# Performance work log

Measured on AMD Instinct MI355X. Metric: run time of the kernel, lower is better.

Reference implementation:

```python
import jax, jax.numpy as jnp
import numpy as np

SLOPE = 0.2
NEG = -9e15

def setup_inputs() -> dict:
    key = jax.random.key(0)
    k1, k2, k3, k4 = jax.random.split(key, 4)
    N, INP, OUT = 8192, 512, 128
    h = jax.random.normal(k1, (N, INP), dtype=jnp.float32)
    adj = jax.random.randint(k2, (N, N), 0, 2, dtype=jnp.int32)
    W = jax.random.normal(k3, (INP, OUT), dtype=jnp.float32) * (1.0 / np.sqrt(INP))
    a = jax.random.normal(k4, (2 * OUT,), dtype=jnp.float32) * (1.0 / np.sqrt(2 * OUT))
    return {"h": h, "adj": adj, "W": W, "a": a}

def reference(h, adj, W, a):
    OUT = W.shape[1]
    Wh = h @ W                               # [N, out]
    # a . [Wh_i, Wh_j] decomposes into two matvecs (same math as pairwise concat)
    f1 = Wh @ a[:OUT]                        # [N]
    f2 = Wh @ a[OUT:]                        # [N]
    e = jax.nn.leaky_relu(f1[:, None] + f2[None, :], negative_slope=SLOPE)  # [N, N]
    scores = jnp.where(adj > 0, e, NEG)
    attention = jax.nn.softmax(scores, axis=1)
    return attention @ Wh                    # [N, out]
```

## Files before the change

kernel.cpp:

```cpp
#include <hip/hip_runtime.h>

typedef unsigned short u16;
typedef __attribute__((ext_vector_type(8))) short short8v;
typedef __attribute__((ext_vector_type(4))) short short4v;
typedef __attribute__((ext_vector_type(4))) float float4v;
typedef __attribute__((ext_vector_type(4))) int   int4v;

#define N_NODES 8192
#define D_IN    512
#define D_OUT   128
#define SLOPEF  0.2f
#define NSEG    4
#define SEGCOLS 2048
#define NCHUNK  8

static __device__ __forceinline__ float bf2f(u16 u) {
    union { unsigned int i; float f; } v; v.i = ((unsigned int)u) << 16; return v.f;
}
static __device__ __forceinline__ u16 f2bf(float f) {
    union { float f; unsigned int i; } v; v.f = f;
    unsigned int r = v.i + 0x7fff + ((v.i >> 16) & 1);
    return (u16)(r >> 16);
}
static __device__ __forceinline__ void lds_barrier() {
    asm volatile("s_waitcnt lgkmcnt(0)" ::: "memory");
    __builtin_amdgcn_s_barrier();
    asm volatile("" ::: "memory");
}

__global__ __launch_bounds__(256, 2) void k1_proj(
        const float* __restrict__ h, const float* __restrict__ W,
        const float* __restrict__ a, u16* __restrict__ WhT,
        float* __restrict__ f1, float* __restrict__ f2)
{
    __shared__ float hs[16 * D_IN];
    __shared__ float buf[16 * 128];
    __shared__ float part[16][17];
    const int tid = threadIdx.x;
    const int rowbase = blockIdx.x * 16;

    const float4v* hsrc = (const float4v*)(h + (size_t)rowbase * D_IN);
    #pragma unroll
    for (int i = 0; i < 8; i++) {
        *(float4v*)&hs[(tid + 256 * i) * 4] = hsrc[tid + 256 * i];
    }
    __syncthreads();

    const int c  = tid & 127;
    const int rh = tid >> 7;
    float acc[8];
    #pragma unroll
    for (int rr = 0; rr < 8; rr++) acc[rr] = 0.f;

    for (int k = 0; k < D_IN; k += 4) {
        float wv[4];
        #pragma unroll
        for (int kk = 0; kk < 4; kk++) wv[kk] = W[(k + kk) * D_OUT + c];
        #pragma unroll
        for (int rr = 0; rr < 8; rr++) {
            float4v hv = *(const float4v*)&hs[(rh * 8 + rr) * D_IN + k];
            acc[rr] += hv[0] * wv[0];
            acc[rr] += hv[1] * wv[1];
            acc[rr] += hv[2] * wv[2];
            acc[rr] += hv[3] * wv[3];
        }
    }

    {
        short8v pack;
        #pragma unroll
        for (int rr = 0; rr < 8; rr++) pack[rr] = (short)f2bf(acc[rr]);
        *(short8v*)(WhT + (size_t)c * N_NODES + rowbase + rh * 8) = pack;
    }

    const float a1 = a[c];
    const float a2 = a[D_OUT + c];

    #pragma unroll
    for (int rr = 0; rr < 8; rr++) buf[(rh * 8 + rr) * 128 + c] = acc[rr] * a1;
    __syncthreads();
    {
        const int row = tid >> 4, seg = tid & 15;
        float p = 0.f;
        #pragma unroll
        for (int e = 0; e < 8; e++) p += buf[row * 128 + seg * 8 + e];
        part[row][seg] = p;
    }
    __syncthreads();
    if (tid < 16) {
        float s = 0.f;
        #pragma unroll
        for (int j = 0; j < 16; j++) s += part[tid][j];
        f1[rowbase + tid] = s;
    }
    __syncthreads();
    #pragma unroll
    for (int rr = 0; rr < 8; rr++) buf[(rh * 8 + rr) * 128 + c] = acc[rr] * a2;
    __syncthreads();
    {
        const int row = tid >> 4, seg = tid & 15;
        float p = 0.f;
        #pragma unroll
        for (int e = 0; e < 8; e++) p += buf[row * 128 + seg * 8 + e];
        part[row][seg] = p;
    }
    __syncthreads();
    if (tid < 16) {
        float s = 0.f;
        #pragma unroll
        for (int j = 0; j < 16; j++) s += part[tid][j];
        f2[rowbase + tid] = s;
    }
}

__global__ __launch_bounds__(256, 4) void k2_attn(
        const int* __restrict__ adj, const u16* __restrict__ WhT,
        const float* __restrict__ f1g, const float* __restrict__ f2g,
        float* __restrict__ numw, float* __restrict__ denw)
{
    __shared__ short Pt[32 * 264];
    __shared__ float f2s[SEGCOLS];
    __shared__ float f1s[32];
    __shared__ float rs[32][9];
    __shared__ float ssum[32];

    const int tid = threadIdx.x;
    const int rb  = blockIdx.x >> 2;
    const int seg = blockIdx.x & 3;
    const int rowbase = rb * 32;
    const int colbase = seg * SEGCOLS;
    const int r = tid >> 3, g = tid & 7;
    const int lane = tid & 63, w = tid >> 6;
    const int quad = lane >> 4, m16 = lane & 15;

    if (tid < 32) f1s[tid] = f1g[rowbase + tid];
    #pragma unroll
    for (int i = 0; i < 2; i++)
        *(float4v*)&f2s[(tid + 256 * i) * 4] = *(const float4v*)&f2g[colbase + (tid + 256 * i) * 4];

    const int4v* arow = (const int4v*)(adj + (size_t)(rowbase + r) * N_NODES + colbase);
    int4v a4[8];
    #pragma unroll
    for (int i = 0; i < 8; i++) a4[i] = arow[g + 8 * i];

    float4v acc[2][2];
    #pragma unroll
    for (int mt = 0; mt < 2; mt++)
        #pragma unroll
        for (int nt = 0; nt < 2; nt++) {
            acc[mt][nt][0] = 0.f; acc[mt][nt][1] = 0.f;
            acc[mt][nt][2] = 0.f; acc[mt][nt][3] = 0.f;
        }
    float lsum = 0.f;

    __syncthreads();

    for (int jc = 0; jc < NCHUNK; jc++) {
        const float f1v = f1s[r];
        #pragma unroll
        for (int i = 0; i < 8; i++) {
            const int c0 = (g + 8 * i) * 4;
            const float4v fv = *(const float4v*)&f2s[jc * 256 + c0];
            const int4v av = a4[i];
            short4v pv;
            #pragma unroll
            for (int e = 0; e < 4; e++) {
                float x = f1v + fv[e];
                x = fmaxf(x, SLOPEF * x);
                const float wv = (av[e] > 0) ? __expf(x) : 0.f;
                const u16 wb = f2bf(wv);
                lsum += bf2f(wb);
                pv[e] = (short)wb;
            }
            *(short4v*)&Pt[r * 264 + c0] = pv;
        }
        if (jc + 1 < NCHUNK) {
            #pragma unroll
            for (int i = 0; i < 8; i++) a4[i] = arow[(jc + 1) * 64 + g + 8 * i];
        }
        lds_barrier();

        {
            const u16* b0p = WhT + (size_t)(w * 32 + m16) * N_NODES + colbase + jc * 256 + quad * 8;
            const u16* b1p = b0p + 16 * N_NODES;
            const short* a0p = &Pt[m16 * 264 + quad * 8];
            const short* a1p = a0p + 16 * 264;
            #pragma unroll
            for (int ks = 0; ks < 8; ks++) {
                const int ko = ks * 32;
                const short8v af0 = *(const short8v*)(a0p + ko);
                const short8v af1 = *(const short8v*)(a1p + ko);
                const short8v bv0 = *(const short8v*)(b0p + ko);
                const short8v bv1 = *(const short8v*)(b1p + ko);
                acc[0][0] = __builtin_amdgcn_mfma_f32_16x16x32_bf16(af0, bv0, acc[0][0], 0, 0, 0);
                acc[0][1] = __builtin_amdgcn_mfma_f32_16x16x32_bf16(af0, bv1, acc[0][1], 0, 0, 0);
                acc[1][0] = __builtin_amdgcn_mfma_f32_16x16x32_bf16(af1, bv0, acc[1][0], 0, 0, 0);
                acc[1][1] = __builtin_amdgcn_mfma_f32_16x16x32_bf16(af1, bv1, acc[1][1], 0, 0, 0);
            }
        }
        lds_barrier();
    }

    rs[r][g] = lsum;
    __syncthreads();
    if (tid < 32) {
        float s = 0.f;
        #pragma unroll
        for (int j = 0; j < 8; j++) s += rs[tid][j];
        ssum[tid] = s;
        denw[(size_t)(rowbase + tid) * NSEG + seg] = s;
    }
    __syncthreads();

    #pragma unroll
    for (int mt = 0; mt < 2; mt++) {
        #pragma unroll
        for (int nt = 0; nt < 2; nt++) {
            const int cl = w * 32 + nt * 16 + m16;
            #pragma unroll
            for (int reg = 0; reg < 4; reg++) {
                const int rl = mt * 16 + quad * 4 + reg;
                numw[((size_t)(rowbase + rl) * NSEG + seg) * D_OUT + cl] = acc[mt][nt][reg];
            }
        }
    }
}

__global__ __launch_bounds__(256) void k3_reduce(
        const float* __restrict__ numw, const float* __restrict__ denw,
        float* __restrict__ out)
{
    const int tid = threadIdx.x;
    const int row = blockIdx.x * 2 + (tid >> 7);
    const int c   = tid & 127;
    float s = 0.f, d = 0.f;
    #pragma unroll
    for (int sg = 0; sg < NSEG; sg++) {
        s += numw[((size_t)row * NSEG + sg) * D_OUT + c];
        d += denw[(size_t)row * NSEG + sg];
    }
    out[(size_t)row * D_OUT + c] = s / d;
}

extern "C" void kernel_launch(void* const* d_in, const int* in_sizes, int n_in,
                              void* d_out, int out_size, void* d_ws, size_t ws_size,
                              hipStream_t stream) {
    const float* h   = (const float*)d_in[0];
    const int*   adj = (const int*)d_in[1];
    const float* W   = (const float*)d_in[2];
    const float* a   = (const float*)d_in[3];

    char* ws = (char*)d_ws;
    u16*   WhT = (u16*)ws;
    float* f1  = (float*)(ws + (size_t)2 * 1024 * 1024);
    float* f2  = f1 + N_NODES;
    float* numw = (float*)(ws + (size_t)4 * 1024 * 1024);
    float* denw = (float*)(ws + (size_t)20 * 1024 * 1024);

    k1_proj<<<N_NODES / 16, 256, 0, stream>>>(h, W, a, WhT, f1, f2);
    k2_attn<<<(N_NODES / 32) * NSEG, 256, 0, stream>>>(adj, WhT, f1, f2, numw, denw);
    k3_reduce<<<N_NODES / 2, 256, 0, stream>>>(numw, denw, (float*)d_out);
}
```

Baseline: 434.1 us.

## Pack adjacency into bitmask in a separate pass and streamline attention weight math

Adds a pre-pass that uses wave ballots to compress the int32 adjacency matrix into a 64-bit-per-word bitmask. The attention kernel then reads one 32-bit mask word per thread per chunk instead of 32 int32 values, and changes the per-thread column mapping so each thread covers 32 contiguous columns with a padded f2 LDS layout. The log2(e) scale is folded into f1/f2 so exp2 can replace exp, and bf16 truncation by bitmask and byte permute replaces round-to-nearest conversion. The adjacency is still read once in full by the pack kernel, so total traffic is unchanged; the gain would have to come from the attention kernel's cheaper inner loop and less register pressure. Truncating to bf16 instead of rounding slightly changes numerics.

```diff
diff --git a/kernel.cpp b/kernel.cpp
--- a/kernel.cpp
+++ b/kernel.cpp
@@ -1,8 +1,8 @@
 #include <hip/hip_runtime.h>
 
 typedef unsigned short u16;
+typedef unsigned int u32;
 typedef __attribute__((ext_vector_type(8))) short short8v;
-typedef __attribute__((ext_vector_type(4))) short short4v;
 typedef __attribute__((ext_vector_type(4))) float float4v;
 typedef __attribute__((ext_vector_type(4))) int   int4v;
 
@@ -10,13 +10,11 @@
 #define D_IN    512
 #define D_OUT   128
 #define SLOPEF  0.2f
+#define LOG2E   1.4426950408889634f
 #define NSEG    4
 #define SEGCOLS 2048
 #define NCHUNK  8
 
-static __device__ __forceinline__ float bf2f(u16 u) {
-    union { unsigned int i; float f; } v; v.i = ((unsigned int)u) << 16; return v.f;
-}
 static __device__ __forceinline__ u16 f2bf(float f) {
     union { float f; unsigned int i; } v; v.f = f;
     unsigned int r = v.i + 0x7fff + ((v.i >> 16) & 1);
@@ -26,6 +24,22 @@
     asm volatile("s_waitcnt lgkmcnt(0)" ::: "memory");
     __builtin_amdgcn_s_barrier();
     asm volatile("" ::: "memory");
+}
+
+__global__ __launch_bounds__(256) void kb_pack(
+        const int* __restrict__ adj, unsigned long long* __restrict__ mask64)
+{
+    const int lane = threadIdx.x & 63;
+    const int gw = (blockIdx.x * 256 + threadIdx.x) >> 6;
+    const int NW = (1024 * 256) / 64;
+    const int NITER = (N_NODES * (N_NODES / 64)) / NW;
+    #pragma unroll 4
+    for (int it = 0; it < NITER; ++it) {
+        const size_t w64 = (size_t)gw + (size_t)NW * it;
+        const int v = adj[w64 * 64 + lane];
+        const unsigned long long b = __ballot(v > 0);
+        if (lane == 0) mask64[w64] = b;
+    }
 }
 
 __global__ __launch_bounds__(256, 2) void k1_proj(
@@ -91,7 +105,7 @@
         float s = 0.f;
         #pragma unroll
         for (int j = 0; j < 16; j++) s += part[tid][j];
-        f1[rowbase + tid] = s;
+        f1[rowbase + tid] = s * LOG2E;
     }
     __syncthreads();
     #pragma unroll
@@ -109,17 +123,17 @@
         float s = 0.f;
         #pragma unroll
         for (int j = 0; j < 16; j++) s += part[tid][j];
-        f2[rowbase + tid] = s;
+        f2[rowbase + tid] = s * LOG2E;
     }
 }
 
 __global__ __launch_bounds__(256, 4) void k2_attn(
-        const int* __restrict__ adj, const u16* __restrict__ WhT,
+        const u32* __restrict__ mask, const u16* __restrict__ WhT,
         const float* __restrict__ f1g, const float* __restrict__ f2g,
         float* __restrict__ numw, float* __restrict__ denw)
 {
     __shared__ short Pt[32 * 264];
-    __shared__ float f2s[SEGCOLS];
+    __shared__ float f2s[2304];
     __shared__ float f1s[32];
     __shared__ float rs[32][9];
     __shared__ float ssum[32];
@@ -135,13 +149,13 @@
 
     if (tid < 32) f1s[tid] = f1g[rowbase + tid];
     #pragma unroll
-    for (int i = 0; i < 2; i++)
-        *(float4v*)&f2s[(tid + 256 * i) * 4] = *(const float4v*)&f2g[colbase + (tid + 256 * i) * 4];
-
-    const int4v* arow = (const int4v*)(adj + (size_t)(rowbase + r) * N_NODES + colbase);
-    int4v a4[8];
-    #pragma unroll
-    for (int i = 0; i < 8; i++) a4[i] = arow[g + 8 * i];
+    for (int i = 0; i < 2; i++) {
+        const int idx = (tid + 256 * i) * 4;
+        *(float4v*)&f2s[idx + ((idx >> 5) << 2)] = *(const float4v*)&f2g[colbase + idx];
+    }
+
+    const u32* mrow = mask + (size_t)(rowbase + r) * (N_NODES / 32) + seg * (SEGCOLS / 32);
+    u32 mcur = mrow[g];
 
     float4v acc[2][2];
     #pragma unroll
@@ -151,33 +165,49 @@
             acc[mt][nt][0] = 0.f; acc[mt][nt][1] = 0.f;
             acc[mt][nt][2] = 0.f; acc[mt][nt][3] = 0.f;
         }
-    float lsum = 0.f;
+    float ls0 = 0.f, ls1 = 0.f, ls2 = 0.f, ls3 = 0.f;
 
     __syncthreads();
 
     for (int jc = 0; jc < NCHUNK; jc++) {
+        u32 mnext = 0;
+        if (jc + 1 < NCHUNK) mnext = mrow[(jc + 1) * 8 + g];
+
         const float f1v = f1s[r];
+        const float* f2p = &f2s[jc * 288 + g * 36];
+        u32 packed[16];
         #pragma unroll
         for (int i = 0; i < 8; i++) {
-            const int c0 = (g + 8 * i) * 4;
-            const float4v fv = *(const float4v*)&f2s[jc * 256 + c0];
-            const int4v av = a4[i];
-            short4v pv;
+            const float4v fv = *(const float4v*)&f2p[i * 4];
+            u32 wb[4];
             #pragma unroll
             for (int e = 0; e < 4; e++) {
+                const int idx = i * 4 + e;
+                const int sel = ((int)(mcur << (31 - idx))) >> 31;
                 float x = f1v + fv[e];
                 x = fmaxf(x, SLOPEF * x);
-                const float wv = (av[e] > 0) ? __expf(x) : 0.f;
-                const u16 wb = f2bf(wv);
-                lsum += bf2f(wb);
-                pv[e] = (short)wb;
-            }
-            *(short4v*)&Pt[r * 264 + c0] = pv;
-        }
-        if (jc + 1 < NCHUNK) {
-            #pragma unroll
-            for (int i = 0; i < 8; i++) a4[i] = arow[(jc + 1) * 64 + g + 8 * i];
-        }
+                const float ex = __builtin_amdgcn_exp2f(x);
+                const u32 wt = __float_as_uint(ex) & ((u32)sel & 0xffff0000u);
+                wb[e] = wt;
+                if (e == 0) ls0 += __uint_as_float(wt);
+                else if (e == 1) ls1 += __uint_as_float(wt);
+                else if (e == 2) ls2 += __uint_as_float(wt);
+                else ls3 += __uint_as_float(wt);
+            }
+            packed[i * 2]     = __builtin_amdgcn_perm(wb[1], wb[0], 0x07060302);
+            packed[i * 2 + 1] = __builtin_amdgcn_perm(wb[3], wb[2], 0x07060302);
+        }
+        {
+            int* pdst = (int*)&Pt[r * 264 + g * 32];
+            #pragma unroll
+            for (int q = 0; q < 4; q++) {
+                int4v st;
+                st[0] = (int)packed[q * 4 + 0]; st[1] = (int)packed[q * 4 + 1];
+                st[2] = (int)packed[q * 4 + 2]; st[3] = (int)packed[q * 4 + 3];
+                *(int4v*)&pdst[q * 4] = st;
+            }
+        }
+        mcur = mnext;
         lds_barrier();
 
         {
@@ -201,7 +231,7 @@
         lds_barrier();
     }
 
-    rs[r][g] = lsum;
+    rs[r][g] = (ls0 + ls1) + (ls2 + ls3);
     __syncthreads();
     if (tid < 32) {
         float s = 0.f;
@@ -251,13 +281,15 @@
     const float* a   = (const float*)d_in[3];
 
     char* ws = (char*)d_ws;
-    u16*   WhT = (u16*)ws;
-    float* f1  = (float*)(ws + (size_t)2 * 1024 * 1024);
+    unsigned long long* mask64 = (unsigned long long*)ws;
+    u16*   WhT = (u16*)(ws + (size_t)8 * 1024 * 1024);
+    float* f1  = (float*)(ws + (size_t)10 * 1024 * 1024);
     float* f2  = f1 + N_NODES;
-    float* numw = (float*)(ws + (size_t)4 * 1024 * 1024);
-    float* denw = (float*)(ws + (size_t)20 * 1024 * 1024);
-
+    float* numw = (float*)(ws + (size_t)12 * 1024 * 1024);
+    float* denw = (float*)(ws + (size_t)28 * 1024 * 1024);
+
+    kb_pack<<<1024, 256, 0, stream>>>(adj, mask64);
     k1_proj<<<N_NODES / 16, 256, 0, stream>>>(h, W, a, WhT, f1, f2);
-    k2_attn<<<(N_NODES / 32) * NSEG, 256, 0, stream>>>(adj, WhT, f1, f2, numw, denw);
+    k2_attn<<<(N_NODES / 32) * NSEG, 256, 0, stream>>>((const u32*)mask64, WhT, f1, f2, numw, denw);
     k3_reduce<<<N_NODES / 2, 256, 0, stream>>>(numw, denw, (float*)d_out);
 }
```

After: 551.1 us. 26.9% more time.
